# Kernel optimization log

Measured on AMD Instinct MI355X. Metric: run time of the kernel, lower is better.

## Reference

```python
import jax, jax.numpy as jnp
import numpy as np

HIDDEN = 2048
N_HEADS = 32
N_KV = 4
HEAD_DIM = 128
EPS = 1e-6
THETA = 1e6
B, S = 2, 2048


def setup_inputs() -> dict:
    key = jax.random.key(0)
    k1, k2, k3 = jax.random.split(key, 3)
    hidden_states = jax.random.normal(k1, (B, S, HIDDEN), dtype=jnp.float32)
    positions = jnp.broadcast_to(jnp.arange(S, dtype=jnp.int32), (B, S))
    w_qkv = jax.random.normal(k2, ((N_HEADS + 2 * N_KV) * HEAD_DIM, HIDDEN), dtype=jnp.float32) * 0.02
    w_o = jax.random.normal(k3, (HIDDEN, N_HEADS * HEAD_DIM), dtype=jnp.float32) * 0.02
    q_norm_w = jnp.ones((HEAD_DIM,), dtype=jnp.float32)
    k_norm_w = jnp.ones((HEAD_DIM,), dtype=jnp.float32)
    return {"hidden_states": hidden_states, "positions": positions,
            "w_qkv": w_qkv, "w_o": w_o, "q_norm_w": q_norm_w, "k_norm_w": k_norm_w}


def _rms_norm(x, w):
    # x: [..., HEAD_DIM]
    var = jnp.mean(x * x, axis=-1, keepdims=True)
    return x * jax.lax.rsqrt(var + EPS) * w


def _rope(x, positions):
    # NEOX-style rotary. x: [B,S,H,D], positions: [B,S]
    half = HEAD_DIM // 2
    inv_freq = 1.0 / (THETA ** (jnp.arange(0, half, dtype=jnp.float32) / half))
    ang = positions.astype(jnp.float32)[..., None] * inv_freq  # [B,S,half]
    cos = jnp.cos(ang)[:, :, None, :]
    sin = jnp.sin(ang)[:, :, None, :]
    x1, x2 = x[..., :half], x[..., half:]
    return jnp.concatenate([x1 * cos - x2 * sin, x2 * cos + x1 * sin], axis=-1)


def reference(hidden_states, positions, w_qkv, w_o, q_norm_w, k_norm_w):
    q_size = N_HEADS * HEAD_DIM
    kv_size = N_KV * HEAD_DIM
    qkv = jnp.einsum('bsh,oh->bso', hidden_states, w_qkv)
    q = qkv[..., :q_size].reshape(B, S, N_HEADS, HEAD_DIM)
    k = qkv[..., q_size:q_size + kv_size].reshape(B, S, N_KV, HEAD_DIM)
    v = qkv[..., q_size + kv_size:].reshape(B, S, N_KV, HEAD_DIM)
    # per-head RMSNorm then RoPE
    q = _rope(_rms_norm(q, q_norm_w), positions)
    k = _rope(_rms_norm(k, k_norm_w), positions)
    rep = N_HEADS // N_KV
    k = jnp.repeat(k, rep, axis=2)
    v = jnp.repeat(v, rep, axis=2)
    scale = HEAD_DIM ** -0.5
    scores = jnp.einsum('bqhd,bkhd->bhqk', q, k) * scale
    causal = jnp.tril(jnp.ones((S, S), dtype=bool))
    scores = jnp.where(causal, scores, jnp.finfo(scores.dtype).min)
    probs = jax.nn.softmax(scores, axis=-1)
    attn = jnp.einsum('bhqk,bkhd->bqhd', probs, v).reshape(B, S, N_HEADS * HEAD_DIM)
    return jnp.einsum('bsa,ha->bsh', attn, w_o)
```

## Files before the change

### kernel.cpp

```cpp
#include <hip/hip_runtime.h>
#include <cstdint>

#define SEQ 2048
#define BATCH 2
#define NTOK 4096
#define HID 2048
#define NH 32
#define NKV 4
#define HD 128
#define QKV_O 5120

typedef __attribute__((ext_vector_type(8))) short short8;
typedef __attribute__((ext_vector_type(8))) unsigned short u16x8;
typedef __attribute__((ext_vector_type(4))) unsigned short u16x4;
typedef __attribute__((ext_vector_type(4))) float f32x4;

__device__ __forceinline__ float bf2f(unsigned short u) {
  union { unsigned int i; float f; } v; v.i = ((unsigned int)u) << 16; return v.f;
}
__device__ __forceinline__ unsigned short f2bf(float f) {
  union { float f; unsigned int i; } v; v.f = f;
  unsigned int r = v.i + 0x7FFFu + ((v.i >> 16) & 1u);
  return (unsigned short)(r >> 16);
}

__device__ __forceinline__ void load_lds16(const void* g, void* l) {
  __builtin_amdgcn_global_load_lds((const __attribute__((address_space(1))) unsigned int*)g,
                                   (__attribute__((address_space(3))) unsigned int*)l, 16, 0, 0);
}

__device__ __forceinline__ float exp2n(float x) { return __builtin_amdgcn_exp2f(x); }

__global__ __launch_bounds__(256) void convert5(
    const float* __restrict__ s0, unsigned short* __restrict__ d0, int n0,
    const float* __restrict__ s1, unsigned short* __restrict__ d1, int n1,
    const float* __restrict__ s2, unsigned short* __restrict__ d2, int n2,
    const float* __restrict__ s3, unsigned short* __restrict__ d3, int n3,
    const float* __restrict__ s4, unsigned short* __restrict__ d4, int n4_) {
  const float* s; unsigned short* d; int n;
  switch (blockIdx.y) {
    case 0: s = s0; d = d0; n = n0; break;
    case 1: s = s1; d = d1; n = n1; break;
    case 2: s = s2; d = d2; n = n2; break;
    case 3: s = s3; d = d3; n = n3; break;
    default: s = s4; d = d4; n = n4_; break;
  }
  int i = blockIdx.x * blockDim.x + threadIdx.x;
  int stride = gridDim.x * blockDim.x;
  for (; i < n; i += stride) {
    f32x4 v = *(const f32x4*)(s + 4 * (size_t)i);
    u16x4 o;
    o.x = f2bf(v.x); o.y = f2bf(v.y); o.z = f2bf(v.z); o.w = f2bf(v.w);
    *(u16x4*)(d + 4 * (size_t)i) = o;
  }
}

__global__ __launch_bounds__(256) void reduce_add(float* __restrict__ out,
                                                  const float* __restrict__ part, int n4) {
  int i = blockIdx.x * blockDim.x + threadIdx.x;
  int stride = gridDim.x * blockDim.x;
  for (; i < n4; i += stride) {
    f32x4 a = *(const f32x4*)(out + 4 * (size_t)i);
    f32x4 b = *(const f32x4*)(part + 4 * (size_t)i);
    a.x += b.x; a.y += b.y; a.z += b.z; a.w += b.w;
    *(f32x4*)(out + 4 * (size_t)i) = a;
  }
}

template <bool OUT_F32, bool SPLIT>
__global__ __launch_bounds__(512, 2) void gemm256(
    const unsigned short* __restrict__ A, const unsigned short* __restrict__ B,
    void* __restrict__ C0, void* __restrict__ C1,
    int lda, int ldb, int ldc, int Kloop) {
  __shared__ alignas(16) unsigned short As[2][256 * 64];
  __shared__ alignas(16) unsigned short Bs[2][256 * 64];

  const int t = threadIdx.x;
  const int lane = t & 63, w = t >> 6;
  const int fr = lane & 15, g = lane >> 4;
  const int wm = w >> 2, wn = w & 3;
  const size_t m0 = (size_t)blockIdx.y * 256;
  const size_t n0 = (size_t)blockIdx.x * 256;
  const int kbase = SPLIT ? (int)blockIdx.z * Kloop : 0;
  void* Cv = (SPLIT && blockIdx.z) ? C1 : C0;

  const int srow = w * 8 + (lane >> 3);
  const int sch = (lane & 7) ^ ((lane >> 3) & 7);
  const unsigned short* gA[4];
  const unsigned short* gB[4];
#pragma unroll
  for (int i = 0; i < 4; i++) {
    gA[i] = A + (m0 + i * 64 + srow) * (size_t)lda + kbase + sch * 8;
    gB[i] = B + (n0 + i * 64 + srow) * (size_t)ldb + kbase + sch * 8;
  }

  auto stage = [&](int k0, int bi) {
#pragma unroll
    for (int i = 0; i < 4; i++) {
      load_lds16(gA[i] + k0, &As[bi][(i * 512 + w * 64) * 8]);
      load_lds16(gB[i] + k0, &Bs[bi][(i * 512 + w * 64) * 8]);
    }
  };

  f32x4 acc[8][4] = {};
  stage(0, 0);

  const int nk = Kloop / 64;
  for (int kt = 0; kt < nk; kt++) {
    const int cur = kt & 1;
    asm volatile("s_waitcnt vmcnt(0)" ::: "memory");
    __builtin_amdgcn_s_barrier();
    __builtin_amdgcn_sched_barrier(0);
    if (kt + 1 < nk) stage((kt + 1) * 64, cur ^ 1);

    const unsigned short* Ac = As[cur];
    const unsigned short* Bc = Bs[cur];

    short8 bfr[4][2];
#pragma unroll
    for (int nf = 0; nf < 4; nf++) {
      const int row = wn * 64 + nf * 16 + fr;
#pragma unroll
      for (int s = 0; s < 2; s++)
        bfr[nf][s] = *(const short8*)&Bc[row * 64 + (((s * 4 + g) ^ (fr & 7)) * 8)];
    }
    __builtin_amdgcn_s_setprio(1);
#pragma unroll
    for (int mf = 0; mf < 8; mf++) {
      const int row = wm * 128 + mf * 16 + fr;
      short8 af0 = *(const short8*)&Ac[row * 64 + (((0 + g) ^ (fr & 7)) * 8)];
      short8 af1 = *(const short8*)&Ac[row * 64 + (((4 + g) ^ (fr & 7)) * 8)];
#pragma unroll
      for (int nf = 0; nf < 4; nf++) {
        acc[mf][nf] = __builtin_amdgcn_mfma_f32_16x16x32_bf16(af0, bfr[nf][0], acc[mf][nf], 0, 0, 0);
        acc[mf][nf] = __builtin_amdgcn_mfma_f32_16x16x32_bf16(af1, bfr[nf][1], acc[mf][nf], 0, 0, 0);
      }
    }
    __builtin_amdgcn_s_setprio(0);
  }

#pragma unroll
  for (int mf = 0; mf < 8; mf++)
#pragma unroll
    for (int nf = 0; nf < 4; nf++) {
      size_t row = m0 + wm * 128 + mf * 16 + g * 4;
      size_t col = n0 + wn * 64 + nf * 16 + fr;
#pragma unroll
      for (int r = 0; r < 4; r++) {
        if (OUT_F32) ((float*)Cv)[(row + r) * ldc + col] = acc[mf][nf][r];
        else ((unsigned short*)Cv)[(row + r) * ldc + col] = f2bf(acc[mf][nf][r]);
      }
    }
}

template <bool OUT_F32>
__global__ __launch_bounds__(256) void gemm_bt_bf16(
    const unsigned short* __restrict__ A, const unsigned short* __restrict__ B,
    void* __restrict__ Cv, int lda, int ldb, int ldc, int K) {
  __shared__ alignas(16) unsigned short As[128 * 32];
  __shared__ alignas(16) unsigned short Bs[128 * 32];

  const int t    = threadIdx.x;
  const int lane = t & 63;
  const int w    = t >> 6;
  const int wm   = (w >> 1) * 64;
  const int wn   = (w & 1) * 64;
  const size_t m0 = (size_t)blockIdx.y * 128;
  const size_t n0 = (size_t)blockIdx.x * 128;

  f32x4 acc[4][4] = {};

  const int srow = w * 32 + (lane >> 2);
  const int scol = (lane & 3) * 8;
  const unsigned short* gA0 = &A[(m0 + srow) * (size_t)lda + scol];
  const unsigned short* gA1 = gA0 + 16 * (size_t)lda;
  const unsigned short* gB0 = &B[(n0 + srow) * (size_t)ldb + scol];
  const unsigned short* gB1 = gB0 + 16 * (size_t)ldb;
  unsigned short* lA0 = &As[(w * 32) * 32];
  unsigned short* lA1 = &As[(w * 32 + 16) * 32];
  unsigned short* lB0 = &Bs[(w * 32) * 32];
  unsigned short* lB1 = &Bs[(w * 32 + 16) * 32];

  const int fr = lane & 15;
  const int kb = (lane >> 4) * 8;

  for (int k0 = 0; k0 < K; k0 += 32) {
    load_lds16(gA0 + k0, lA0);
    load_lds16(gA1 + k0, lA1);
    load_lds16(gB0 + k0, lB0);
    load_lds16(gB1 + k0, lB1);
    __syncthreads();
    short8 af[4], bf[4];
#pragma unroll
    for (int mt = 0; mt < 4; mt++) af[mt] = *(const short8*)&As[(wm + mt * 16 + fr) * 32 + kb];
#pragma unroll
    for (int nt = 0; nt < 4; nt++) bf[nt] = *(const short8*)&Bs[(wn + nt * 16 + fr) * 32 + kb];
#pragma unroll
    for (int mt = 0; mt < 4; mt++)
#pragma unroll
      for (int nt = 0; nt < 4; nt++)
        acc[mt][nt] = __builtin_amdgcn_mfma_f32_16x16x32_bf16(af[mt], bf[nt], acc[mt][nt], 0, 0, 0);
    __syncthreads();
  }

  const int r4 = (lane >> 4) * 4;
  const int cc = lane & 15;
#pragma unroll
  for (int mt = 0; mt < 4; mt++)
#pragma unroll
    for (int nt = 0; nt < 4; nt++) {
      size_t row = m0 + wm + mt * 16 + r4;
      size_t col = n0 + wn + nt * 16 + cc;
#pragma unroll
      for (int r = 0; r < 4; r++) {
        if (OUT_F32) ((float*)Cv)[(row + r) * ldc + col] = acc[mt][nt][r];
        else ((unsigned short*)Cv)[(row + r) * ldc + col] = f2bf(acc[mt][nt][r]);
      }
    }
}

__global__ __launch_bounds__(64) void rope_tab(const int* __restrict__ pos,
                                               float2* __restrict__ tab) {
  const int tok = blockIdx.x;
  const int j = threadIdx.x;
  float p = (float)pos[tok];
  float inv_freq = expf((float)j * (-13.815510557964274f / 64.0f));
  float ang = p * inv_freq;
  float2 cs; cs.x = cosf(ang); cs.y = sinf(ang);
  tab[tok * 64 + j] = cs;
}

__global__ __launch_bounds__(256) void normrope(
    unsigned short* __restrict__ qkv, const float2* __restrict__ tab,
    const unsigned short* __restrict__ qw, const unsigned short* __restrict__ kw) {
  const int wv   = threadIdx.x >> 6;
  const int lane = threadIdx.x & 63;
  const int h    = blockIdx.x * 4 + wv;
  const int tok  = blockIdx.z * SEQ + blockIdx.y;

  const unsigned short* w = (h < NH) ? qw : kw;
  const size_t src = (size_t)tok * QKV_O + (size_t)h * HD;

  float x1 = bf2f(qkv[src + lane]);
  float x2 = bf2f(qkv[src + lane + 64]);
  float ss = x1 * x1 + x2 * x2;
#pragma unroll
  for (int off = 32; off; off >>= 1) ss += __shfl_xor(ss, off);
  float r = rsqrtf(ss * (1.0f / 128.0f) + 1e-6f);
  float n1 = x1 * r * bf2f(w[lane]);
  float n2 = x2 * r * bf2f(w[lane + 64]);

  float2 cs = tab[tok * 64 + lane];
  qkv[src + lane]      = f2bf(n1 * cs.x - n2 * cs.y);
  qkv[src + lane + 64] = f2bf(n2 * cs.x + n1 * cs.y);
}

__global__ __launch_bounds__(256) void transpose_v(const unsigned short* __restrict__ qkv,
                                                   unsigned short* __restrict__ vt) {
  __shared__ alignas(16) unsigned short Vs[64][136];
  const int k0 = blockIdx.x * 64, kvh = blockIdx.y, b = blockIdx.z;
  const int t = threadIdx.x;
  const int voff = (NH + NKV) * HD + kvh * HD;
  {
    const int row = t >> 2, cb = (t & 3) * 8;
    const size_t gb = (size_t)(b * SEQ + k0 + row) * QKV_O + voff;
#pragma unroll
    for (int r = 0; r < 4; r++)
      *(uint4*)&Vs[row][cb + 32 * r] = *(const uint4*)&qkv[gb + cb + 32 * r];
  }
  __syncthreads();
  const int d = t >> 1, half = t & 1;
  const size_t ob = ((size_t)((b * NKV + kvh) * HD + d)) * SEQ + k0 + half * 32;
#pragma unroll
  for (int i = 0; i < 4; i++) {
    u16x8 vv;
#pragma unroll
    for (int j = 0; j < 8; j++) vv[j] = Vs[half * 32 + i * 8 + j][d];
    *(u16x8*)&vt[ob + i * 8] = vv;
  }
}

__global__ __launch_bounds__(512, 4) void flash_mfma(unsigned short* __restrict__ qkv,
                                                     const unsigned short* __restrict__ vt) {
  __shared__ alignas(16) unsigned short Kbuf[2][64 * 128];
  __shared__ alignas(16) unsigned short Vbuf[2][128 * 64];
  __shared__ alignas(16) unsigned short Ps[8][16 * 64];

  const int p = (int)blockIdx.x;
  const int h = blockIdx.y, b = blockIdx.z;
  const int t = threadIdx.x;
  const int lane = t & 63, w = t >> 6;
  const int c = lane & 15, g = lane >> 4;
  const int kvh = h >> 3;
  const int koff = NH * HD + kvh * HD;
  const float scale2 = 0.12751745f;
  const int swz = c & 7;
  const int nqt = SEQ / 128;

  const int rK0 = t >> 4,         jK0 = (t & 15) ^ (rK0 & 15);
  const int rK1 = (t + 512) >> 4, jK1 = ((t + 512) & 15) ^ (rK1 & 15);
  const int dV0 = t >> 3,         jV0 = (t & 7) ^ (dV0 & 7);
  const int dV1 = (t + 512) >> 3, jV1 = ((t + 512) & 7) ^ (dV1 & 7);
  const unsigned short* gK0 = qkv + (size_t)(b * SEQ + rK0) * QKV_O + koff + jK0 * 8;
  const unsigned short* gK1 = qkv + (size_t)(b * SEQ + rK1) * QKV_O + koff + jK1 * 8;
  const unsigned short* gV0 = vt + ((size_t)(b * NKV + kvh) * HD + dV0) * SEQ + jV0 * 8;
  const unsigned short* gV1 = vt + ((size_t)(b * NKV + kvh) * HD + dV1) * SEQ + jV1 * 8;

  auto stage = [&](int k0s, int bi) {
    load_lds16(gK0 + (size_t)k0s * QKV_O, &Kbuf[bi][(w * 64) * 8]);
    load_lds16(gK1 + (size_t)k0s * QKV_O, &Kbuf[bi][(w * 64 + 512) * 8]);
    load_lds16(gV0 + k0s, &Vbuf[bi][(w * 64) * 8]);
    load_lds16(gV1 + k0s, &Vbuf[bi][(w * 64 + 512) * 8]);
  };

  for (int job = 0; job < 2; job++) {
    const int qt = job == 0 ? (nqt - 1 - p) : p;
    const int q0 = qt * 128;
    const int nkt = 2 * qt + 2;

    stage(0, 0);

    short8 qf[4];
    {
      const size_t qr = (size_t)(b * SEQ + q0 + w * 16 + c) * QKV_O + (size_t)h * HD;
#pragma unroll
      for (int ks = 0; ks < 4; ks++)
        qf[ks] = *(const short8*)&qkv[qr + ks * 32 + g * 8];
    }

    f32x4 O[8] = {};
    float m_i = -1e30f, l_i = 0.0f;

    for (int kt = 0; kt < nkt; kt++) {
      const int cur = kt & 1;
      asm volatile("s_waitcnt vmcnt(0)" ::: "memory");
      __builtin_amdgcn_s_barrier();
      __builtin_amdgcn_sched_barrier(0);
      if (kt + 1 < nkt) stage((kt + 1) * 64, cur ^ 1);

      const unsigned short* Kc = Kbuf[cur];
      const unsigned short* Vc = Vbuf[cur];

      f32x4 sc[4];
#pragma unroll
      for (int mt = 0; mt < 4; mt++) sc[mt] = (f32x4){0.f, 0.f, 0.f, 0.f};
      __builtin_amdgcn_s_setprio(1);
#pragma unroll
      for (int ks = 0; ks < 4; ks++) {
#pragma unroll
        for (int mt = 0; mt < 4; mt++) {
          short8 kf = *(const short8*)&Kc[(mt * 16 + c) * 128 + (((ks * 4 + g) ^ c) * 8)];
          sc[mt] = __builtin_amdgcn_mfma_f32_16x16x32_bf16(kf, qf[ks], sc[mt], 0, 0, 0);
        }
      }
      __builtin_amdgcn_s_setprio(0);

      const int k0 = kt * 64;
      const int qrow = q0 + w * 16 + c;
      const bool need_mask = (k0 + 63 > q0 + w * 16);
#pragma unroll
      for (int mt = 0; mt < 4; mt++)
#pragma unroll
        for (int r = 0; r < 4; r++) {
          float s = sc[mt][r];
          if (need_mask && (k0 + mt * 16 + g * 4 + r > qrow)) s = -3.0e38f;
          sc[mt][r] = s;
        }
      float ma = fmaxf(fmaxf(sc[0][0], sc[0][1]), sc[0][2]);
      float mb = fmaxf(fmaxf(sc[0][3], sc[1][0]), sc[1][1]);
      float mc = fmaxf(fmaxf(sc[1][2], sc[1][3]), sc[2][0]);
      float md = fmaxf(fmaxf(sc[2][1], sc[2][2]), sc[2][3]);
      float me = fmaxf(fmaxf(sc[3][0], sc[3][1]), sc[3][2]);
      float mx = fmaxf(fmaxf(fmaxf(ma, mb), fmaxf(mc, md)), fmaxf(me, sc[3][3]));
      mx = fmaxf(mx, __shfl_xor(mx, 16));
      mx = fmaxf(mx, __shfl_xor(mx, 32));
      float mx2 = mx * scale2;

      if (!__all(mx2 - m_i <= 11.54156f)) {
        float m_new = fmaxf(m_i, mx2);
        float alpha = exp2n(m_i - m_new);
        f32x4 a4;
#pragma unroll
        for (int r = 0; r < 4; r++) a4[r] = __shfl(alpha, g * 4 + r);
#pragma unroll
        for (int nt = 0; nt < 8; nt++)
#pragma unroll
          for (int r = 0; r < 4; r++) O[nt][r] *= a4[r];
        l_i *= alpha;
        m_i = m_new;
      }

      float psum = 0.0f;
#pragma unroll
      for (int mt = 0; mt < 4; mt++) {
        float pv[4];
#pragma unroll
        for (int r = 0; r < 4; r++) {
          pv[r] = exp2n(__builtin_fmaf(sc[mt][r], scale2, -m_i));
          psum += pv[r];
        }
        unsigned int pk0, pk1;
        asm("v_cvt_pk_bf16_f32 %0, %1, %2" : "=v"(pk0) : "v"(pv[0]), "v"(pv[1]));
        asm("v_cvt_pk_bf16_f32 %0, %1, %2" : "=v"(pk1) : "v"(pv[2]), "v"(pv[3]));
        uint2 pk; pk.x = pk0; pk.y = pk1;
        *(uint2*)&Ps[w][c * 64 + (((mt * 2 + (g >> 1)) ^ swz) * 8) + (g & 1) * 4] = pk;
      }
      psum += __shfl_xor(psum, 16);
      psum += __shfl_xor(psum, 32);
      l_i += psum;

      __builtin_amdgcn_s_setprio(1);
#pragma unroll
      for (int ks = 0; ks < 2; ks++) {
        short8 pf = *(const short8*)&Ps[w][c * 64 + (((ks * 4 + g) ^ swz) * 8)];
#pragma unroll
        for (int nt = 0; nt < 8; nt++) {
          short8 vf = *(const short8*)&Vc[(nt * 16 + c) * 64 + (((ks * 4 + g) ^ swz) * 8)];
          O[nt] = __builtin_amdgcn_mfma_f32_16x16x32_bf16(pf, vf, O[nt], 0, 0, 0);
        }
      }
      __builtin_amdgcn_s_setprio(0);
    }

    f32x4 l4;
#pragma unroll
    for (int r = 0; r < 4; r++) l4[r] = __shfl(l_i, g * 4 + r);
    f32x4 li;
#pragma unroll
    for (int r = 0; r < 4; r++) li[r] = 1.0f / l4[r];
#pragma unroll
    for (int nt = 0; nt < 8; nt++)
#pragma unroll
      for (int r = 0; r < 4; r++) {
        size_t addr = (size_t)(b * SEQ + q0 + w * 16 + g * 4 + r) * QKV_O + h * HD + nt * 16 + c;
        qkv[addr] = f2bf(O[nt][r] * li[r]);
      }
  }
}

extern "C" void kernel_launch(void* const* d_in, const int* in_sizes, int n_in,
                              void* d_out, int out_size, void* d_ws, size_t ws_size,
                              hipStream_t stream) {
  const float* hidden_f = (const float*)d_in[0];
  const int* positions  = (const int*)d_in[1];
  const float* wqkv_f   = (const float*)d_in[2];
  const float* wo_f     = (const float*)d_in[3];
  const float* qn_f     = (const float*)d_in[4];
  const float* kn_f     = (const float*)d_in[5];
  float* out            = (float*)d_out;

  char* ws = (char*)d_ws;
  unsigned short* hidden_c = (unsigned short*)ws;
  unsigned short* wqkv_c   = (unsigned short*)(ws + 16777216);
  unsigned short* wo_c     = (unsigned short*)(ws + 37748736);
  unsigned short* qn_c     = (unsigned short*)(ws + 54525952);
  unsigned short* kn_c     = (unsigned short*)(ws + 54526208);
  unsigned short* qkv      = (unsigned short*)(ws + 54526464);
  unsigned short* vt_g     = (unsigned short*)(ws + 96469504);
  float2* rtab             = (float2*)ws;
  float* p0                = (float*)ws;

  convert5<<<dim3(512, 5), 256, 0, stream>>>(
      hidden_f, hidden_c, NTOK * HID / 4,
      wqkv_f, wqkv_c, QKV_O * HID / 4,
      wo_f, wo_c, HID * NH * HD / 4,
      qn_f, qn_c, HD / 4,
      kn_f, kn_c, HD / 4);

  gemm256<false, false><<<dim3(NH * HD / 256, NTOK / 256), 512, 0, stream>>>(
      hidden_c, wqkv_c, qkv, qkv, HID, HID, QKV_O, HID);
  gemm_bt_bf16<false><<<dim3(2 * NKV * HD / 128, NTOK / 128), 256, 0, stream>>>(
      hidden_c, wqkv_c + (size_t)(NH * HD) * HID, qkv + NH * HD, HID, HID, QKV_O, HID);
  rope_tab<<<NTOK, 64, 0, stream>>>(positions, rtab);
  normrope<<<dim3((NH + NKV) / 4, SEQ, BATCH), 256, 0, stream>>>(qkv, rtab, qn_c, kn_c);
  transpose_v<<<dim3(SEQ / 64, NKV, BATCH), 256, 0, stream>>>(qkv, vt_g);
  flash_mfma<<<dim3(SEQ / 256, NH, BATCH), 512, 0, stream>>>(qkv, vt_g);
  gemm256<true, true><<<dim3(HID / 256, NTOK / 256, 2), 512, 0, stream>>>(
      qkv, wo_c, p0, out, QKV_O, NH * HD, HID, NH * HD / 2);
  reduce_add<<<2048, 256, 0, stream>>>(out, p0, NTOK * HID / 4);
}
```

Measured before the change: 477.0 us.

## Replace split-K output projection with single-pass 256x128 tiled GEMM

```diff
diff --git a/kernel.cpp b/kernel.cpp
--- a/kernel.cpp
+++ b/kernel.cpp
@@ -55,23 +55,10 @@
   }
 }
 
-__global__ __launch_bounds__(256) void reduce_add(float* __restrict__ out,
-                                                  const float* __restrict__ part, int n4) {
-  int i = blockIdx.x * blockDim.x + threadIdx.x;
-  int stride = gridDim.x * blockDim.x;
-  for (; i < n4; i += stride) {
-    f32x4 a = *(const f32x4*)(out + 4 * (size_t)i);
-    f32x4 b = *(const f32x4*)(part + 4 * (size_t)i);
-    a.x += b.x; a.y += b.y; a.z += b.z; a.w += b.w;
-    *(f32x4*)(out + 4 * (size_t)i) = a;
-  }
-}
-
-template <bool OUT_F32, bool SPLIT>
+template <bool OUT_F32>
 __global__ __launch_bounds__(512, 2) void gemm256(
     const unsigned short* __restrict__ A, const unsigned short* __restrict__ B,
-    void* __restrict__ C0, void* __restrict__ C1,
-    int lda, int ldb, int ldc, int Kloop) {
+    void* __restrict__ Cv, int lda, int ldb, int ldc, int Kloop) {
   __shared__ alignas(16) unsigned short As[2][256 * 64];
   __shared__ alignas(16) unsigned short Bs[2][256 * 64];
 
@@ -81,8 +68,6 @@
   const int wm = w >> 2, wn = w & 3;
   const size_t m0 = (size_t)blockIdx.y * 256;
   const size_t n0 = (size_t)blockIdx.x * 256;
-  const int kbase = SPLIT ? (int)blockIdx.z * Kloop : 0;
-  void* Cv = (SPLIT && blockIdx.z) ? C1 : C0;
 
   const int srow = w * 8 + (lane >> 3);
   const int sch = (lane & 7) ^ ((lane >> 3) & 7);
@@ -90,8 +75,8 @@
   const unsigned short* gB[4];
 #pragma unroll
   for (int i = 0; i < 4; i++) {
-    gA[i] = A + (m0 + i * 64 + srow) * (size_t)lda + kbase + sch * 8;
-    gB[i] = B + (n0 + i * 64 + srow) * (size_t)ldb + kbase + sch * 8;
+    gA[i] = A + (m0 + i * 64 + srow) * (size_t)lda + sch * 8;
+    gB[i] = B + (n0 + i * 64 + srow) * (size_t)ldb + sch * 8;
   }
 
   auto stage = [&](int k0, int bi) {
@@ -150,6 +135,88 @@
         if (OUT_F32) ((float*)Cv)[(row + r) * ldc + col] = acc[mf][nf][r];
         else ((unsigned short*)Cv)[(row + r) * ldc + col] = f2bf(acc[mf][nf][r]);
       }
+    }
+}
+
+__global__ __launch_bounds__(512, 2) void gemm256x128(
+    const unsigned short* __restrict__ A, const unsigned short* __restrict__ B,
+    float* __restrict__ C, int lda, int ldb, int ldc, int Kloop) {
+  __shared__ alignas(16) unsigned short As[2][256 * 64];
+  __shared__ alignas(16) unsigned short Bs[2][128 * 64];
+
+  const int t = threadIdx.x;
+  const int lane = t & 63, w = t >> 6;
+  const int fr = lane & 15, g = lane >> 4;
+  const int wm = w >> 1, wn = w & 1;
+  const size_t m0 = (size_t)blockIdx.y * 256;
+  const size_t n0 = (size_t)blockIdx.x * 128;
+
+  const int srow = t >> 3;
+  const int sch = (t & 7) ^ ((t >> 3) & 7);
+  const unsigned short* gA[4];
+  const unsigned short* gB[2];
+#pragma unroll
+  for (int i = 0; i < 4; i++)
+    gA[i] = A + (m0 + i * 64 + srow) * (size_t)lda + sch * 8;
+#pragma unroll
+  for (int i = 0; i < 2; i++)
+    gB[i] = B + (n0 + i * 64 + srow) * (size_t)ldb + sch * 8;
+
+  auto stage = [&](int k0, int bi) {
+#pragma unroll
+    for (int i = 0; i < 4; i++)
+      load_lds16(gA[i] + k0, &As[bi][(i * 512 + w * 64) * 8]);
+#pragma unroll
+    for (int i = 0; i < 2; i++)
+      load_lds16(gB[i] + k0, &Bs[bi][(i * 512 + w * 64) * 8]);
+  };
+
+  f32x4 acc[4][4] = {};
+  stage(0, 0);
+
+  const int nk = Kloop / 64;
+  for (int kt = 0; kt < nk; kt++) {
+    const int cur = kt & 1;
+    asm volatile("s_waitcnt vmcnt(0)" ::: "memory");
+    __builtin_amdgcn_s_barrier();
+    __builtin_amdgcn_sched_barrier(0);
+    if (kt + 1 < nk) stage((kt + 1) * 64, cur ^ 1);
+
+    const unsigned short* Ac = As[cur];
+    const unsigned short* Bc = Bs[cur];
+
+    short8 bfr[4][2];
+#pragma unroll
+    for (int nf = 0; nf < 4; nf++) {
+      const int row = wn * 64 + nf * 16 + fr;
+#pragma unroll
+      for (int s = 0; s < 2; s++)
+        bfr[nf][s] = *(const short8*)&Bc[row * 64 + (((s * 4 + g) ^ (fr & 7)) * 8)];
+    }
+    __builtin_amdgcn_s_setprio(1);
+#pragma unroll
+    for (int mf = 0; mf < 4; mf++) {
+      const int row = wm * 64 + mf * 16 + fr;
+      short8 af0 = *(const short8*)&Ac[row * 64 + (((0 + g) ^ (fr & 7)) * 8)];
+      short8 af1 = *(const short8*)&Ac[row * 64 + (((4 + g) ^ (fr & 7)) * 8)];
+#pragma unroll
+      for (int nf = 0; nf < 4; nf++) {
+        acc[mf][nf] = __builtin_amdgcn_mfma_f32_16x16x32_bf16(af0, bfr[nf][0], acc[mf][nf], 0, 0, 0);
+        acc[mf][nf] = __builtin_amdgcn_mfma_f32_16x16x32_bf16(af1, bfr[nf][1], acc[mf][nf], 0, 0, 0);
+      }
+    }
+    __builtin_amdgcn_s_setprio(0);
+  }
+
+#pragma unroll
+  for (int mf = 0; mf < 4; mf++)
+#pragma unroll
+    for (int nf = 0; nf < 4; nf++) {
+      size_t row = m0 + wm * 64 + mf * 16 + g * 4;
+      size_t col = n0 + wn * 64 + nf * 16 + fr;
+#pragma unroll
+      for (int r = 0; r < 4; r++)
+        C[(row + r) * ldc + col] = acc[mf][nf][r];
     }
 }
 
@@ -458,7 +525,6 @@
   unsigned short* qkv      = (unsigned short*)(ws + 54526464);
   unsigned short* vt_g     = (unsigned short*)(ws + 96469504);
   float2* rtab             = (float2*)ws;
-  float* p0                = (float*)ws;
 
   convert5<<<dim3(512, 5), 256, 0, stream>>>(
       hidden_f, hidden_c, NTOK * HID / 4,
@@ -467,15 +533,14 @@
       qn_f, qn_c, HD / 4,
       kn_f, kn_c, HD / 4);
 
-  gemm256<false, false><<<dim3(NH * HD / 256, NTOK / 256), 512, 0, stream>>>(
-      hidden_c, wqkv_c, qkv, qkv, HID, HID, QKV_O, HID);
+  gemm256<false><<<dim3(NH * HD / 256, NTOK / 256), 512, 0, stream>>>(
+      hidden_c, wqkv_c, qkv, HID, HID, QKV_O, HID);
   gemm_bt_bf16<false><<<dim3(2 * NKV * HD / 128, NTOK / 128), 256, 0, stream>>>(
       hidden_c, wqkv_c + (size_t)(NH * HD) * HID, qkv + NH * HD, HID, HID, QKV_O, HID);
   rope_tab<<<NTOK, 64, 0, stream>>>(positions, rtab);
   normrope<<<dim3((NH + NKV) / 4, SEQ, BATCH), 256, 0, stream>>>(qkv, rtab, qn_c, kn_c);
   transpose_v<<<dim3(SEQ / 64, NKV, BATCH), 256, 0, stream>>>(qkv, vt_g);
   flash_mfma<<<dim3(SEQ / 256, NH, BATCH), 512, 0, stream>>>(qkv, vt_g);
-  gemm256<true, true><<<dim3(HID / 256, NTOK / 256, 2), 512, 0, stream>>>(
-      qkv, wo_c, p0, out, QKV_O, NH * HD, HID, NH * HD / 2);
-  reduce_add<<<2048, 256, 0, stream>>>(out, p0, NTOK * HID / 4);
-}
+  gemm256x128<<<dim3(HID / 128, NTOK / 256), 512, 0, stream>>>(
+      qkv, wo_c, out, QKV_O, NH * HD, HID, NH * HD);
+}
```

Result: no change. 472.2 us (-1.0%).

## Restructure 256x256 GEMM into four-phase ping-pong with staggered half-tile loads

Applied to the files above, without the earlier changes.

```diff
diff --git a/kernel.cpp b/kernel.cpp
--- a/kernel.cpp
+++ b/kernel.cpp
@@ -68,7 +68,7 @@
 }
 
 template <bool OUT_F32, bool SPLIT>
-__global__ __launch_bounds__(512, 2) void gemm256(
+__global__ __launch_bounds__(512, 2) void gemm256_8p(
     const unsigned short* __restrict__ A, const unsigned short* __restrict__ B,
     void* __restrict__ C0, void* __restrict__ C1,
     int lda, int ldb, int ldc, int Kloop) {
@@ -78,7 +78,8 @@
   const int t = threadIdx.x;
   const int lane = t & 63, w = t >> 6;
   const int fr = lane & 15, g = lane >> 4;
-  const int wm = w >> 2, wn = w & 3;
+  const int wr = (w >> 2) * 64;
+  const int wc = (w & 3) * 32;
   const size_t m0 = (size_t)blockIdx.y * 256;
   const size_t n0 = (size_t)blockIdx.x * 256;
   const int kbase = SPLIT ? (int)blockIdx.z * Kloop : 0;
@@ -94,63 +95,126 @@
     gB[i] = B + (n0 + i * 64 + srow) * (size_t)ldb + kbase + sch * 8;
   }
 
-  auto stage = [&](int k0, int bi) {
-#pragma unroll
-    for (int i = 0; i < 4; i++) {
-      load_lds16(gA[i] + k0, &As[bi][(i * 512 + w * 64) * 8]);
-      load_lds16(gB[i] + k0, &Bs[bi][(i * 512 + w * 64) * 8]);
-    }
+  auto stA = [&](int half, int k0, int bi) {
+    load_lds16(gA[2 * half] + k0,     &As[bi][(half * 1024 + w * 64) * 8]);
+    load_lds16(gA[2 * half + 1] + k0, &As[bi][(half * 1024 + 512 + w * 64) * 8]);
   };
-
-  f32x4 acc[8][4] = {};
-  stage(0, 0);
-
+  auto stB = [&](int half, int k0, int bi) {
+    load_lds16(gB[2 * half] + k0,     &Bs[bi][(half * 1024 + w * 64) * 8]);
+    load_lds16(gB[2 * half + 1] + k0, &Bs[bi][(half * 1024 + 512 + w * 64) * 8]);
+  };
+
+  const int ck0 = ((0 + g) ^ (fr & 7)) * 8;
+  const int ck1 = ((4 + g) ^ (fr & 7)) * 8;
+
+  f32x4 acc[4][4][2] = {};
   const int nk = Kloop / 64;
+
+  stA(0, 0, 0); stB(0, 0, 0); stB(1, 0, 0); stA(1, 0, 0);
+  if (nk > 1) { stA(0, 64, 1); stB(0, 64, 1); }
+
   for (int kt = 0; kt < nk; kt++) {
     const int cur = kt & 1;
-    asm volatile("s_waitcnt vmcnt(0)" ::: "memory");
+    const unsigned short* Ac = As[cur];
+    const unsigned short* Bc = Bs[cur];
+    const int kn1 = (kt + 1) * 64, kn2 = (kt + 2) * 64;
+
+    if (kt + 1 < nk) asm volatile("s_waitcnt vmcnt(4)" ::: "memory");
+    else             asm volatile("s_waitcnt vmcnt(0)" ::: "memory");
     __builtin_amdgcn_s_barrier();
     __builtin_amdgcn_sched_barrier(0);
-    if (kt + 1 < nk) stage((kt + 1) * 64, cur ^ 1);
-
-    const unsigned short* Ac = As[cur];
-    const unsigned short* Bc = Bs[cur];
-
-    short8 bfr[4][2];
-#pragma unroll
-    for (int nf = 0; nf < 4; nf++) {
-      const int row = wn * 64 + nf * 16 + fr;
-#pragma unroll
-      for (int s = 0; s < 2; s++)
-        bfr[nf][s] = *(const short8*)&Bc[row * 64 + (((s * 4 + g) ^ (fr & 7)) * 8)];
+
+    short8 Af[4][2], Bf0[2][2], Bf1[2][2];
+
+    if (kt + 1 < nk) stB(1, kn1, cur ^ 1);
+#pragma unroll
+    for (int mf = 0; mf < 4; mf++) {
+      Af[mf][0] = *(const short8*)&Ac[(wr + mf * 16 + fr) * 64 + ck0];
+      Af[mf][1] = *(const short8*)&Ac[(wr + mf * 16 + fr) * 64 + ck1];
+    }
+#pragma unroll
+    for (int nf = 0; nf < 2; nf++) {
+      Bf0[nf][0] = *(const short8*)&Bc[(wc + nf * 16 + fr) * 64 + ck0];
+      Bf0[nf][1] = *(const short8*)&Bc[(wc + nf * 16 + fr) * 64 + ck1];
     }
     __builtin_amdgcn_s_setprio(1);
 #pragma unroll
-    for (int mf = 0; mf < 8; mf++) {
-      const int row = wm * 128 + mf * 16 + fr;
-      short8 af0 = *(const short8*)&Ac[row * 64 + (((0 + g) ^ (fr & 7)) * 8)];
-      short8 af1 = *(const short8*)&Ac[row * 64 + (((4 + g) ^ (fr & 7)) * 8)];
-#pragma unroll
-      for (int nf = 0; nf < 4; nf++) {
-        acc[mf][nf] = __builtin_amdgcn_mfma_f32_16x16x32_bf16(af0, bfr[nf][0], acc[mf][nf], 0, 0, 0);
-        acc[mf][nf] = __builtin_amdgcn_mfma_f32_16x16x32_bf16(af1, bfr[nf][1], acc[mf][nf], 0, 0, 0);
-      }
-    }
+    for (int mf = 0; mf < 4; mf++)
+#pragma unroll
+      for (int nf = 0; nf < 2; nf++) {
+        acc[0][mf][nf] = __builtin_amdgcn_mfma_f32_16x16x32_bf16(Af[mf][0], Bf0[nf][0], acc[0][mf][nf], 0, 0, 0);
+        acc[0][mf][nf] = __builtin_amdgcn_mfma_f32_16x16x32_bf16(Af[mf][1], Bf0[nf][1], acc[0][mf][nf], 0, 0, 0);
+      }
     __builtin_amdgcn_s_setprio(0);
-  }
-
-#pragma unroll
-  for (int mf = 0; mf < 8; mf++)
-#pragma unroll
-    for (int nf = 0; nf < 4; nf++) {
-      size_t row = m0 + wm * 128 + mf * 16 + g * 4;
-      size_t col = n0 + wn * 64 + nf * 16 + fr;
-#pragma unroll
-      for (int r = 0; r < 4; r++) {
-        if (OUT_F32) ((float*)Cv)[(row + r) * ldc + col] = acc[mf][nf][r];
-        else ((unsigned short*)Cv)[(row + r) * ldc + col] = f2bf(acc[mf][nf][r]);
-      }
-    }
+    __builtin_amdgcn_s_barrier();
+    __builtin_amdgcn_sched_barrier(0);
+
+    if (kt + 1 < nk) stA(1, kn1, cur ^ 1);
+#pragma unroll
+    for (int nf = 0; nf < 2; nf++) {
+      Bf1[nf][0] = *(const short8*)&Bc[(128 + wc + nf * 16 + fr) * 64 + ck0];
+      Bf1[nf][1] = *(const short8*)&Bc[(128 + wc + nf * 16 + fr) * 64 + ck1];
+    }
+    __builtin_amdgcn_s_setprio(1);
+#pragma unroll
+    for (int mf = 0; mf < 4; mf++)
+#pragma unroll
+      for (int nf = 0; nf < 2; nf++) {
+        acc[1][mf][nf] = __builtin_amdgcn_mfma_f32_16x16x32_bf16(Af[mf][0], Bf1[nf][0], acc[1][mf][nf], 0, 0, 0);
+        acc[1][mf][nf] = __builtin_amdgcn_mfma_f32_16x16x32_bf16(Af[mf][1], Bf1[nf][1], acc[1][mf][nf], 0, 0, 0);
+      }
+    __builtin_amdgcn_s_setprio(0);
+    __builtin_amdgcn_s_barrier();
+    __builtin_amdgcn_sched_barrier(0);
+
+    if (kt + 2 < nk) stA(0, kn2, cur);
+#pragma unroll
+    for (int mf = 0; mf < 4; mf++) {
+      Af[mf][0] = *(const short8*)&Ac[(128 + wr + mf * 16 + fr) * 64 + ck0];
+      Af[mf][1] = *(const short8*)&Ac[(128 + wr + mf * 16 + fr) * 64 + ck1];
+    }
+    __builtin_amdgcn_s_setprio(1);
+#pragma unroll
+    for (int mf = 0; mf < 4; mf++)
+#pragma unroll
+      for (int nf = 0; nf < 2; nf++) {
+        acc[2][mf][nf] = __builtin_amdgcn_mfma_f32_16x16x32_bf16(Af[mf][0], Bf0[nf][0], acc[2][mf][nf], 0, 0, 0);
+        acc[2][mf][nf] = __builtin_amdgcn_mfma_f32_16x16x32_bf16(Af[mf][1], Bf0[nf][1], acc[2][mf][nf], 0, 0, 0);
+      }
+    __builtin_amdgcn_s_setprio(0);
+    __builtin_amdgcn_s_barrier();
+    __builtin_amdgcn_sched_barrier(0);
+
+    if (kt + 2 < nk) stB(0, kn2, cur);
+    __builtin_amdgcn_s_setprio(1);
+#pragma unroll
+    for (int mf = 0; mf < 4; mf++)
+#pragma unroll
+      for (int nf = 0; nf < 2; nf++) {
+        acc[3][mf][nf] = __builtin_amdgcn_mfma_f32_16x16x32_bf16(Af[mf][0], Bf1[nf][0], acc[3][mf][nf], 0, 0, 0);
+        acc[3][mf][nf] = __builtin_amdgcn_mfma_f32_16x16x32_bf16(Af[mf][1], Bf1[nf][1], acc[3][mf][nf], 0, 0, 0);
+      }
+    __builtin_amdgcn_s_setprio(0);
+    __builtin_amdgcn_s_barrier();
+    __builtin_amdgcn_sched_barrier(0);
+  }
+
+#pragma unroll
+  for (int q = 0; q < 4; q++) {
+    const int Qm = q >> 1, Qn = q & 1;
+#pragma unroll
+    for (int mf = 0; mf < 4; mf++)
+#pragma unroll
+      for (int nf = 0; nf < 2; nf++) {
+        size_t row = m0 + Qm * 128 + wr + mf * 16 + g * 4;
+        size_t col = n0 + Qn * 128 + wc + nf * 16 + fr;
+#pragma unroll
+        for (int r = 0; r < 4; r++) {
+          if (OUT_F32) ((float*)Cv)[(row + r) * ldc + col] = acc[q][mf][nf][r];
+          else ((unsigned short*)Cv)[(row + r) * ldc + col] = f2bf(acc[q][mf][nf][r]);
+        }
+      }
+  }
 }
 
 template <bool OUT_F32>
@@ -467,7 +531,7 @@
       qn_f, qn_c, HD / 4,
       kn_f, kn_c, HD / 4);
 
-  gemm256<false, false><<<dim3(NH * HD / 256, NTOK / 256), 512, 0, stream>>>(
+  gemm256_8p<false, false><<<dim3(NH * HD / 256, NTOK / 256), 512, 0, stream>>>(
       hidden_c, wqkv_c, qkv, qkv, HID, HID, QKV_O, HID);
   gemm_bt_bf16<false><<<dim3(2 * NKV * HD / 128, NTOK / 128), 256, 0, stream>>>(
       hidden_c, wqkv_c + (size_t)(NH * HD) * HID, qkv + NH * HD, HID, HID, QKV_O, HID);
@@ -475,7 +539,7 @@
   normrope<<<dim3((NH + NKV) / 4, SEQ, BATCH), 256, 0, stream>>>(qkv, rtab, qn_c, kn_c);
   transpose_v<<<dim3(SEQ / 64, NKV, BATCH), 256, 0, stream>>>(qkv, vt_g);
   flash_mfma<<<dim3(SEQ / 256, NH, BATCH), 512, 0, stream>>>(qkv, vt_g);
-  gemm256<true, true><<<dim3(HID / 256, NTOK / 256, 2), 512, 0, stream>>>(
+  gemm256_8p<true, true><<<dim3(HID / 256, NTOK / 256, 2), 512, 0, stream>>>(
       qkv, wo_c, p0, out, QKV_O, NH * HD, HID, NH * HD / 2);
   reduce_add<<<2048, 256, 0, stream>>>(out, p0, NTOK * HID / 4);
 }
```

Result: slower. 500.8 us (+5.0%).

## Restructure 256x256 GEMM into 8-phase quadrant schedule with interleaved LDS staging

Applied to the files above, without the earlier changes.

```diff
diff --git a/kernel.cpp b/kernel.cpp
--- a/kernel.cpp
+++ b/kernel.cpp
@@ -68,7 +68,7 @@
 }
 
 template <bool OUT_F32, bool SPLIT>
-__global__ __launch_bounds__(512, 2) void gemm256(
+__global__ __launch_bounds__(512, 2) void gemm256_8p(
     const unsigned short* __restrict__ A, const unsigned short* __restrict__ B,
     void* __restrict__ C0, void* __restrict__ C1,
     int lda, int ldb, int ldc, int Kloop) {
@@ -78,7 +78,8 @@
   const int t = threadIdx.x;
   const int lane = t & 63, w = t >> 6;
   const int fr = lane & 15, g = lane >> 4;
-  const int wm = w >> 2, wn = w & 3;
+  const int wr = (w >> 2) * 64;
+  const int wc = (w & 3) * 32;
   const size_t m0 = (size_t)blockIdx.y * 256;
   const size_t n0 = (size_t)blockIdx.x * 256;
   const int kbase = SPLIT ? (int)blockIdx.z * Kloop : 0;
@@ -94,63 +95,117 @@
     gB[i] = B + (n0 + i * 64 + srow) * (size_t)ldb + kbase + sch * 8;
   }
 
-  auto stage = [&](int k0, int bi) {
-#pragma unroll
-    for (int i = 0; i < 4; i++) {
-      load_lds16(gA[i] + k0, &As[bi][(i * 512 + w * 64) * 8]);
-      load_lds16(gB[i] + k0, &Bs[bi][(i * 512 + w * 64) * 8]);
+  auto stA = [&](int half, int k0, int bi) {
+    load_lds16(gA[2 * half] + k0,     &As[bi][(half * 1024 + w * 64) * 8]);
+    load_lds16(gA[2 * half + 1] + k0, &As[bi][(half * 1024 + 512 + w * 64) * 8]);
+  };
+  auto stB = [&](int half, int k0, int bi) {
+    load_lds16(gB[2 * half] + k0,     &Bs[bi][(half * 1024 + w * 64) * 8]);
+    load_lds16(gB[2 * half + 1] + k0, &Bs[bi][(half * 1024 + 512 + w * 64) * 8]);
+  };
+
+  const int ck0 = ((0 + g) ^ (fr & 7)) * 8;
+  const int ck1 = ((4 + g) ^ (fr & 7)) * 8;
+
+  f32x4 acc0[4][2] = {}, acc1[4][2] = {}, acc2[4][2] = {}, acc3[4][2] = {};
+  const int nk = Kloop / 64;
+  const int niter = nk / 2;
+
+#define RD_A(BASE, HOFF)                                                      \
+  _Pragma("unroll")                                                           \
+  for (int mf = 0; mf < 4; mf++) {                                            \
+    Af[mf][0] = *(const short8*)&BASE[(HOFF + wr + mf * 16 + fr) * 64 + ck0]; \
+    Af[mf][1] = *(const short8*)&BASE[(HOFF + wr + mf * 16 + fr) * 64 + ck1]; \
+  }
+#define RD_B(BASE, HOFF)                                                      \
+  _Pragma("unroll")                                                           \
+  for (int nf = 0; nf < 2; nf++) {                                            \
+    Bf[nf][0] = *(const short8*)&BASE[(HOFF + wc + nf * 16 + fr) * 64 + ck0]; \
+    Bf[nf][1] = *(const short8*)&BASE[(HOFF + wc + nf * 16 + fr) * 64 + ck1]; \
+  }
+#define MMA_QUAD(ACCQ)                                                        \
+  __builtin_amdgcn_s_setprio(1);                                              \
+  _Pragma("unroll")                                                           \
+  for (int mf = 0; mf < 4; mf++)                                              \
+    _Pragma("unroll")                                                         \
+    for (int nf = 0; nf < 2; nf++) {                                          \
+      ACCQ[mf][nf] = __builtin_amdgcn_mfma_f32_16x16x32_bf16(Af[mf][0], Bf[nf][0], ACCQ[mf][nf], 0, 0, 0); \
+      ACCQ[mf][nf] = __builtin_amdgcn_mfma_f32_16x16x32_bf16(Af[mf][1], Bf[nf][1], ACCQ[mf][nf], 0, 0, 0); \
+    }                                                                         \
+  __builtin_amdgcn_s_setprio(0);
+#define BAR1 __builtin_amdgcn_s_barrier();
+#define BAR2 __builtin_amdgcn_s_barrier(); __builtin_amdgcn_sched_barrier(0);
+
+  stA(0, 0, 0); stA(1, 0, 0); stB(0, 0, 0); stB(1, 0, 0);
+  stA(0, 64, 1); stB(1, 64, 1); stA(1, 64, 1);
+  asm volatile("s_waitcnt vmcnt(6)" ::: "memory");
+  BAR2
+
+  const unsigned short* A0c = As[0]; const unsigned short* B0c = Bs[0];
+  const unsigned short* A1c = As[1]; const unsigned short* B1c = Bs[1];
+
+  for (int it = 0; it < niter; it++) {
+    const int kt = 2 * it;
+    const bool last = (it == niter - 1);
+    const int kT1 = (kt + 1) * 64, kT2 = (kt + 2) * 64, kT3 = (kt + 3) * 64;
+    short8 Af[4][2], Bf[2][2];
+
+    RD_A(A0c, 0) RD_B(B0c, 0)
+    stB(0, kT1, 1);
+    BAR1 MMA_QUAD(acc0) BAR2
+    RD_B(B0c, 128)
+    if (!last) stA(0, kT2, 0);
+    BAR1 MMA_QUAD(acc1) BAR2
+    RD_A(A0c, 128)
+    if (!last) stB(1, kT2, 0);
+    BAR1 MMA_QUAD(acc2) BAR2
+    RD_B(B0c, 0)
+    if (!last) stA(1, kT2, 0);
+    BAR1 MMA_QUAD(acc3)
+    if (last) asm volatile("s_waitcnt vmcnt(0)" ::: "memory");
+    else      asm volatile("s_waitcnt vmcnt(6)" ::: "memory");
+    BAR2
+    RD_A(A1c, 0) RD_B(B1c, 0)
+    if (!last) stB(0, kT2, 0);
+    BAR1 MMA_QUAD(acc0) BAR2
+    RD_B(B1c, 128)
+    if (kt + 3 < nk) stA(0, kT3, 1);
+    BAR1 MMA_QUAD(acc1) BAR2
+    RD_A(A1c, 128)
+    if (kt + 3 < nk) stB(1, kT3, 1);
+    BAR1 MMA_QUAD(acc2) BAR2
+    RD_B(B1c, 0)
+    if (kt + 3 < nk) stA(1, kT3, 1);
+    BAR1 MMA_QUAD(acc3)
+    if (!last) asm volatile("s_waitcnt vmcnt(6)" ::: "memory");
+    BAR2
+  }
+
+#define STORE_Q(ACCQ, RQ, CQ)                                                 \
+  _Pragma("unroll")                                                           \
+  for (int mf = 0; mf < 4; mf++)                                              \
+    _Pragma("unroll")                                                         \
+    for (int nf = 0; nf < 2; nf++) {                                          \
+      size_t row = m0 + RQ + wr + mf * 16 + g * 4;                            \
+      size_t col = n0 + CQ + wc + nf * 16 + fr;                               \
+      _Pragma("unroll")                                                       \
+      for (int r = 0; r < 4; r++) {                                           \
+        if (OUT_F32) ((float*)Cv)[(row + r) * ldc + col] = ACCQ[mf][nf][r];   \
+        else ((unsigned short*)Cv)[(row + r) * ldc + col] = f2bf(ACCQ[mf][nf][r]); \
+      }                                                                       \
     }
-  };
-
-  f32x4 acc[8][4] = {};
-  stage(0, 0);
-
-  const int nk = Kloop / 64;
-  for (int kt = 0; kt < nk; kt++) {
-    const int cur = kt & 1;
-    asm volatile("s_waitcnt vmcnt(0)" ::: "memory");
-    __builtin_amdgcn_s_barrier();
-    __builtin_amdgcn_sched_barrier(0);
-    if (kt + 1 < nk) stage((kt + 1) * 64, cur ^ 1);
-
-    const unsigned short* Ac = As[cur];
-    const unsigned short* Bc = Bs[cur];
-
-    short8 bfr[4][2];
-#pragma unroll
-    for (int nf = 0; nf < 4; nf++) {
-      const int row = wn * 64 + nf * 16 + fr;
-#pragma unroll
-      for (int s = 0; s < 2; s++)
-        bfr[nf][s] = *(const short8*)&Bc[row * 64 + (((s * 4 + g) ^ (fr & 7)) * 8)];
-    }
-    __builtin_amdgcn_s_setprio(1);
-#pragma unroll
-    for (int mf = 0; mf < 8; mf++) {
-      const int row = wm * 128 + mf * 16 + fr;
-      short8 af0 = *(const short8*)&Ac[row * 64 + (((0 + g) ^ (fr & 7)) * 8)];
-      short8 af1 = *(const short8*)&Ac[row * 64 + (((4 + g) ^ (fr & 7)) * 8)];
-#pragma unroll
-      for (int nf = 0; nf < 4; nf++) {
-        acc[mf][nf] = __builtin_amdgcn_mfma_f32_16x16x32_bf16(af0, bfr[nf][0], acc[mf][nf], 0, 0, 0);
-        acc[mf][nf] = __builtin_amdgcn_mfma_f32_16x16x32_bf16(af1, bfr[nf][1], acc[mf][nf], 0, 0, 0);
-      }
-    }
-    __builtin_amdgcn_s_setprio(0);
-  }
-
-#pragma unroll
-  for (int mf = 0; mf < 8; mf++)
-#pragma unroll
-    for (int nf = 0; nf < 4; nf++) {
-      size_t row = m0 + wm * 128 + mf * 16 + g * 4;
-      size_t col = n0 + wn * 64 + nf * 16 + fr;
-#pragma unroll
-      for (int r = 0; r < 4; r++) {
-        if (OUT_F32) ((float*)Cv)[(row + r) * ldc + col] = acc[mf][nf][r];
-        else ((unsigned short*)Cv)[(row + r) * ldc + col] = f2bf(acc[mf][nf][r]);
-      }
-    }
+
+  STORE_Q(acc0, 0, 0)
+  STORE_Q(acc1, 0, 128)
+  STORE_Q(acc2, 128, 128)
+  STORE_Q(acc3, 128, 0)
+
+#undef RD_A
+#undef RD_B
+#undef MMA_QUAD
+#undef BAR1
+#undef BAR2
+#undef STORE_Q
 }
 
 template <bool OUT_F32>
@@ -467,7 +522,7 @@
       qn_f, qn_c, HD / 4,
       kn_f, kn_c, HD / 4);
 
-  gemm256<false, false><<<dim3(NH * HD / 256, NTOK / 256), 512, 0, stream>>>(
+  gemm256_8p<false, false><<<dim3(NH * HD / 256, NTOK / 256), 512, 0, stream>>>(
       hidden_c, wqkv_c, qkv, qkv, HID, HID, QKV_O, HID);
   gemm_bt_bf16<false><<<dim3(2 * NKV * HD / 128, NTOK / 128), 256, 0, stream>>>(
       hidden_c, wqkv_c + (size_t)(NH * HD) * HID, qkv + NH * HD, HID, HID, QKV_O, HID);
@@ -475,7 +530,7 @@
   normrope<<<dim3((NH + NKV) / 4, SEQ, BATCH), 256, 0, stream>>>(qkv, rtab, qn_c, kn_c);
   transpose_v<<<dim3(SEQ / 64, NKV, BATCH), 256, 0, stream>>>(qkv, vt_g);
   flash_mfma<<<dim3(SEQ / 256, NH, BATCH), 512, 0, stream>>>(qkv, vt_g);
-  gemm256<true, true><<<dim3(HID / 256, NTOK / 256, 2), 512, 0, stream>>>(
+  gemm256_8p<true, true><<<dim3(HID / 256, NTOK / 256, 2), 512, 0, stream>>>(
       qkv, wo_c, p0, out, QKV_O, NH * HD, HID, NH * HD / 2);
   reduce_add<<<2048, 256, 0, stream>>>(out, p0, NTOK * HID / 4);
 }
```

After: 479.4 us. About the same (+0.5%).
